# Kernel optimization log

Hardware: AMD Instinct MI355X
Metric: run time of the kernel (lower is better)

The kernel has to match this reference:

```python
import jax, jax.numpy as jnp
import numpy as np

N_NODES = 100000
NEG_SLOPE = 0.2  # PyG GATConv default leaky_relu slope


def gat_conv(x, src, dst, W, a_src, a_dst, b, concat):
    # x: [N, F_in], W: [F_in, H*C], a_src/a_dst: [H, C], b: [H*C] or [C]
    N = x.shape[0]
    H, C = a_src.shape
    h = (x @ W).reshape(N, H, C)                       # [N, H, C]
    alpha_s = jnp.einsum('nhc,hc->nh', h, a_src)       # [N, H]
    alpha_d = jnp.einsum('nhc,hc->nh', h, a_dst)       # [N, H]
    e = jax.nn.leaky_relu(alpha_s[src] + alpha_d[dst], NEG_SLOPE)  # [E, H]
    # edge-softmax grouped by destination node (numerically stable)
    e_max = jax.ops.segment_max(e, dst, num_segments=N)            # [N, H]
    e_exp = jnp.exp(e - e_max[dst])
    denom = jax.ops.segment_sum(e_exp, dst, num_segments=N)        # [N, H]
    alpha = e_exp / (denom[dst] + 1e-16)                           # [E, H]
    msg = h[src] * alpha[:, :, None]                               # [E, H, C]
    out = jax.ops.segment_sum(msg, dst, num_segments=N)            # [N, H, C]
    out = out.reshape(N, H * C) if concat else out.mean(axis=1)
    return out + b


def setup_inputs() -> dict:
    key = jax.random.key(0)
    ks = jax.random.split(key, 12)
    in_dim, hidden, heads, out_dim = 512, 128, 4, 64
    c1 = hidden // heads   # 32 per-head channels, concat -> hidden
    c2 = hidden            # 128 per-head channels, mean over heads
    E = 600000
    x = jax.random.normal(ks[0], (N_NODES, in_dim), dtype=jnp.float32)
    edge_index = jax.random.randint(ks[1], (2, E), 0, N_NODES, dtype=jnp.int64)
    s = 0.1
    return {
        'x': x,
        'edge_index': edge_index,
        'W1': jax.random.normal(ks[2], (in_dim, heads * c1), dtype=jnp.float32) * s,
        'a_src1': jax.random.normal(ks[3], (heads, c1), dtype=jnp.float32) * s,
        'a_dst1': jax.random.normal(ks[4], (heads, c1), dtype=jnp.float32) * s,
        'b1': jnp.zeros((heads * c1,), dtype=jnp.float32),
        'W2': jax.random.normal(ks[5], (hidden, heads * c2), dtype=jnp.float32) * s,
        'a_src2': jax.random.normal(ks[6], (heads, c2), dtype=jnp.float32) * s,
        'a_dst2': jax.random.normal(ks[7], (heads, c2), dtype=jnp.float32) * s,
        'b2': jnp.zeros((c2,), dtype=jnp.float32),
        'W_lin': jax.random.normal(ks[8], (hidden, out_dim), dtype=jnp.float32) * s,
        'b_lin': jnp.zeros((out_dim,), dtype=jnp.float32),
    }


def reference(x, edge_index, W1, a_src1, a_dst1, b1, W2, a_src2, a_dst2, b2, W_lin, b_lin):
    N = x.shape[0]
    # add self-loops (PyG GATConv default add_self_loops=True)
    loops = jnp.arange(N, dtype=edge_index.dtype)
    src = jnp.concatenate([edge_index[0], loops])
    dst = jnp.concatenate([edge_index[1], loops])
    # dropout layers are identity at inference (training=False)
    h = gat_conv(x, src, dst, W1, a_src1, a_dst1, b1, concat=True)
    h = jax.nn.elu(h)
    embeddings = gat_conv(h, src, dst, W2, a_src2, a_dst2, b2, concat=False)
    out = embeddings @ W_lin + b_lin
    return out, embeddings
```

## Files before the change

kernel.cpp:

```cpp
#include <hip/hip_runtime.h>
#include <hip/hip_bf16.h>

typedef __hip_bfloat16 bf16;
typedef unsigned short u16;
typedef unsigned int u32;
typedef u16 u16x8 __attribute__((ext_vector_type(8)));
typedef __bf16 bf16x8 __attribute__((ext_vector_type(8)));
typedef float f32x4 __attribute__((ext_vector_type(4)));

__device__ __forceinline__ float tof(float x) { return x; }
__device__ __forceinline__ float tof(bf16 x) { return __bfloat162float(x); }
__device__ __forceinline__ bf16 tobf(float x) { return __float2bfloat16(x); }

__device__ __forceinline__ u16 f2bf(float x) {
    unsigned u = __builtin_bit_cast(unsigned, x);
    u += 0x7fffu + ((u >> 16) & 1u);
    return (u16)(u >> 16);
}
__device__ __forceinline__ float bf2f(u16 h) {
    return __builtin_bit_cast(float, (unsigned)h << 16);
}
__device__ __forceinline__ float bflo(u32 u) {
    return __builtin_bit_cast(float, u << 16);
}
__device__ __forceinline__ float bfhi(u32 u) {
    return __builtin_bit_cast(float, u & 0xffff0000u);
}
__device__ __forceinline__ void cstore(u16* p, float v) { *p = f2bf(v); }
__device__ __forceinline__ void cstore(float* p, float v) { *p = v; }

__global__ void tsplit_k(const float* __restrict__ W, int K, int N,
                         u16* __restrict__ hi, u16* __restrict__ lo)
{
    int i = blockIdx.x * blockDim.x + threadIdx.x;
    if (i >= K * N) return;
    int k = i / N, n = i - k * N;
    float v = W[i];
    u16 h = f2bf(v);
    hi[(long)n * K + k] = h;
    lo[(long)n * K + k] = f2bf(v - bf2f(h));
}

__global__ void tsplit2_k(const float* __restrict__ W2,
                          u16* __restrict__ hi, u16* __restrict__ lo)
{
    int i = blockIdx.x * blockDim.x + threadIdx.x;
    if (i >= 128 * 512) return;
    int c = i >> 9, o2 = i & 511;
    int hh = o2 >> 7, o = o2 & 127;
    float v = W2[i];
    u16 h = f2bf(v);
    long dsti = (long)o * 512 + hh * 128 + c;
    hi[dsti] = h;
    lo[dsti] = f2bf(v - bf2f(h));
}

__global__ void vmat_k(const float* __restrict__ W2, const float* __restrict__ as2,
                       const float* __restrict__ ad2,
                       float* __restrict__ Vs, float* __restrict__ Vd)
{
    int i = blockIdx.x * blockDim.x + threadIdx.x;
    if (i >= 512) return;
    int hh = i >> 7, c = i & 127;
    float s = 0.f, d = 0.f;
    const float* wrow = W2 + (long)c * 512 + hh * 128;
    const float* ar = as2 + hh * 128;
    const float* br = ad2 + hh * 128;
    for (int o = 0; o < 128; ++o) {
        float w = wrow[o];
        s += w * ar[o];
        d += w * br[o];
    }
    Vs[i] = s;
    Vd[i] = d;
}

template <bool SPLIT_A, typename TC>
__global__ __launch_bounds__(256) void gemm_mfma(
    const void* __restrict__ Avoid, const u16* __restrict__ Bhi,
    const u16* __restrict__ Blo, TC* __restrict__ C,
    int M, int Ntot, int K, const float* __restrict__ bias)
{
    __shared__ u16 AsHi[128 * 64];
    __shared__ u16 AsLo[SPLIT_A ? 128 * 64 : 8];
    __shared__ u16 BsHi[128 * 64];
    __shared__ u16 BsLo[128 * 64];
    const int t = threadIdx.x;
    const long bm = (long)blockIdx.y * 128;
    const int bn = blockIdx.x * 128;
    const int srow = t >> 1;
    const int skh  = t & 1;
    const int w  = t >> 6;
    const int wm = (w >> 1) * 64;
    const int wn = (w & 1) * 64;
    const int l  = t & 63;
    const int lr = l & 15;
    const int lg = l >> 4;

    f32x4 acc[4][4];
#pragma unroll
    for (int i = 0; i < 4; ++i)
#pragma unroll
        for (int j = 0; j < 4; ++j) acc[i][j] = {0.f, 0.f, 0.f, 0.f};

    for (int k0 = 0; k0 < K; k0 += 64) {
        {
            long r = bm + srow;
            bool ok = r < M;
            if (SPLIT_A) {
                const float* A = (const float*)Avoid;
                const float4* ap = (const float4*)(A + r * K + k0 + skh * 32);
#pragma unroll
                for (int c = 0; c < 4; ++c) {
                    float va[8];
                    if (ok) {
                        float4 v0 = ap[c * 2], v1 = ap[c * 2 + 1];
                        va[0] = v0.x; va[1] = v0.y; va[2] = v0.z; va[3] = v0.w;
                        va[4] = v1.x; va[5] = v1.y; va[6] = v1.z; va[7] = v1.w;
                    } else {
#pragma unroll
                        for (int j = 0; j < 8; ++j) va[j] = 0.f;
                    }
                    u16x8 hi, lo;
#pragma unroll
                    for (int j = 0; j < 8; ++j) {
                        u16 h = f2bf(va[j]);
                        hi[j] = h;
                        lo[j] = f2bf(va[j] - bf2f(h));
                    }
                    int off = srow * 128 + ((((skh * 4 + c) ^ (srow & 7))) << 4);
                    *(u16x8*)((char*)AsHi + off) = hi;
                    *(u16x8*)((char*)AsLo + off) = lo;
                }
            } else {
                const u16* A = (const u16*)Avoid;
                const u16x8* ap = (const u16x8*)(A + r * K + k0 + skh * 32);
#pragma unroll
                for (int c = 0; c < 4; ++c) {
                    u16x8 hv = {0, 0, 0, 0, 0, 0, 0, 0};
                    if (ok) hv = ap[c];
                    int off = srow * 128 + ((((skh * 4 + c) ^ (srow & 7))) << 4);
                    *(u16x8*)((char*)AsHi + off) = hv;
                }
            }
        }
        {
            const u16x8* bph = (const u16x8*)(Bhi + (long)(bn + srow) * K + k0 + skh * 32);
            const u16x8* bpl = (const u16x8*)(Blo + (long)(bn + srow) * K + k0 + skh * 32);
#pragma unroll
            for (int c = 0; c < 4; ++c) {
                int off = srow * 128 + ((((skh * 4 + c) ^ (srow & 7))) << 4);
                *(u16x8*)((char*)BsHi + off) = bph[c];
                *(u16x8*)((char*)BsLo + off) = bpl[c];
            }
        }
        __syncthreads();
#pragma unroll
        for (int ks = 0; ks < 2; ++ks) {
            bf16x8 bh[4], bl[4];
            const int chl = ks * 4 + lg;
#pragma unroll
            for (int n = 0; n < 4; ++n) {
                int col = wn + n * 16 + lr;
                int off = col * 128 + (((chl ^ (col & 7))) << 4);
                bh[n] = *(const bf16x8*)((const char*)BsHi + off);
                bl[n] = *(const bf16x8*)((const char*)BsLo + off);
            }
#pragma unroll
            for (int m = 0; m < 4; ++m) {
                int row = wm + m * 16 + lr;
                int off = row * 128 + (((chl ^ (row & 7))) << 4);
                bf16x8 ah = *(const bf16x8*)((const char*)AsHi + off);
#pragma unroll
                for (int n = 0; n < 4; ++n)
                    acc[m][n] = __builtin_amdgcn_mfma_f32_16x16x32_bf16(
                        ah, bh[n], acc[m][n], 0, 0, 0);
#pragma unroll
                for (int n = 0; n < 4; ++n)
                    acc[m][n] = __builtin_amdgcn_mfma_f32_16x16x32_bf16(
                        ah, bl[n], acc[m][n], 0, 0, 0);
                if (SPLIT_A) {
                    bf16x8 al = *(const bf16x8*)((const char*)AsLo + off);
#pragma unroll
                    for (int n = 0; n < 4; ++n)
                        acc[m][n] = __builtin_amdgcn_mfma_f32_16x16x32_bf16(
                            al, bh[n], acc[m][n], 0, 0, 0);
                }
            }
        }
        __syncthreads();
    }
#pragma unroll
    for (int m = 0; m < 4; ++m) {
        long r0 = bm + wm + m * 16 + lg * 4;
#pragma unroll
        for (int i = 0; i < 4; ++i) {
            long r = r0 + i;
            if (r < M) {
#pragma unroll
                for (int n = 0; n < 4; ++n) {
                    int col = bn + wn + n * 16 + lr;
                    float v = acc[m][n][i];
                    if (bias) v += bias[col];
                    cstore(&C[r * Ntot + col], v);
                }
            }
        }
    }
}

__global__ void alpha4_k(const bf16* __restrict__ h, const float* __restrict__ asrc,
                         const float* __restrict__ adst, float* __restrict__ out_s,
                         float* __restrict__ out_d, int N)
{
    int i = blockIdx.x * blockDim.x + threadIdx.x;
    if (i >= N * 4) return;
    int n = i >> 2, hh = i & 3;
    const bf16* row = h + (long)n * 128 + hh * 32;
    const float* av = asrc + hh * 32;
    const float* bv = adst + hh * 32;
    float s1 = 0.f, s2 = 0.f;
    for (int c = 0; c < 32; ++c) {
        float v = tof(row[c]);
        s1 += v * av[c];
        s2 += v * bv[c];
    }
    out_s[i] = s1;
    out_d[i] = s2;
}

__global__ void alpha2v_k(const bf16* __restrict__ out1b, const float* __restrict__ Vs,
                          const float* __restrict__ Vd, float* __restrict__ out_s,
                          float* __restrict__ out_d, int N)
{
    int i = blockIdx.x * blockDim.x + threadIdx.x;
    if (i >= N * 4) return;
    int n = i >> 2, hh = i & 3;
    const u32* rp = (const u32*)((const u16*)out1b + (long)n * 128);
    const float* vs = Vs + hh * 128;
    const float* vd = Vd + hh * 128;
    float s1 = 0.f, s2 = 0.f;
#pragma unroll 8
    for (int c2 = 0; c2 < 64; ++c2) {
        u32 u = rp[c2];
        float lo = bflo(u), hi = bfhi(u);
        s1 += lo * vs[c2 * 2] + hi * vs[c2 * 2 + 1];
        s2 += lo * vd[c2 * 2] + hi * vd[c2 * 2 + 1];
    }
    out_s[i] = s1;
    out_d[i] = s2;
}

__global__ void init_cnt_k(int* __restrict__ cnt, int N)
{
    int i = blockIdx.x * blockDim.x + threadIdx.x;
    if (i < N) cnt[i] = 1;
}

__global__ void hist_k(const int* __restrict__ dst, int E, int* __restrict__ cnt)
{
    int e = blockIdx.x * blockDim.x + threadIdx.x;
    if (e < E) atomicAdd(&cnt[dst[e]], 1);
}

__global__ __launch_bounds__(256) void scan_blk_k(const int* __restrict__ cnt,
                                                  int* __restrict__ row_ptr,
                                                  int* __restrict__ bsum, int N)
{
    __shared__ int s[256];
    int t = threadIdx.x;
    int i = blockIdx.x * 256 + t;
    int v = (i < N) ? cnt[i] : 0;
    s[t] = v;
    __syncthreads();
    for (int off = 1; off < 256; off <<= 1) {
        int x = (t >= off) ? s[t - off] : 0;
        __syncthreads();
        s[t] += x;
        __syncthreads();
    }
    if (i < N) row_ptr[i] = s[t] - v;
    if (t == 255) bsum[blockIdx.x] = s[255];
}

__global__ __launch_bounds__(512) void scan_top_k(const int* __restrict__ bsum,
                                                  int* __restrict__ bofs, int B)
{
    __shared__ int s[512];
    int t = threadIdx.x;
    int v = (t < B) ? bsum[t] : 0;
    s[t] = v;
    __syncthreads();
    for (int off = 1; off < 512; off <<= 1) {
        int x = (t >= off) ? s[t - off] : 0;
        __syncthreads();
        s[t] += x;
        __syncthreads();
    }
    bofs[t] = s[t] - v;
}

__global__ void add_off_k(int* __restrict__ row_ptr, const int* __restrict__ bofs,
                          int* __restrict__ wofs, int N, int Etot)
{
    int i = blockIdx.x * blockDim.x + threadIdx.x;
    if (i == 0) row_ptr[N] = Etot;
    if (i >= N) return;
    int r = row_ptr[i] + bofs[i >> 8];
    row_ptr[i] = r;
    wofs[i] = r;
}

__global__ void scatter_k(const int* __restrict__ dst, const int* __restrict__ src,
                          int E, int Etot,
                          int* __restrict__ wofs, int* __restrict__ sidx)
{
    int e = blockIdx.x * blockDim.x + threadIdx.x;
    if (e >= Etot) return;
    int d, s;
    if (e < E) { d = dst[e]; s = src[e]; }
    else       { d = e - E;  s = d; }
    int pos = atomicAdd(&wofs[d], 1);
    sidx[pos] = s;
}

__global__ void edgew_k(const int* __restrict__ row_ptr, const int* __restrict__ sidx,
                        const float* __restrict__ asv, const float* __restrict__ adv,
                        float* __restrict__ aw, float* __restrict__ invden, int N)
{
    int i = blockIdx.x * blockDim.x + threadIdx.x;
    if (i >= N * 4) return;
    int d = i >> 2, hh = i & 3;
    int beg = row_ptr[d], end = row_ptr[d + 1];
    float ad_d = adv[i];
    float m = -1e30f;
    for (int j = beg; j < end; ++j) {
        float l = asv[sidx[j] * 4 + hh] + ad_d;
        l = l > 0.f ? l : 0.2f * l;
        m = fmaxf(m, l);
    }
    float den = 0.f;
    for (int j = beg; j < end; ++j) {
        float l = asv[sidx[j] * 4 + hh] + ad_d;
        l = l > 0.f ? l : 0.2f * l;
        float w = __expf(l - m);
        den += w;
        aw[(long)j * 4 + hh] = w;
    }
    invden[i] = 1.f / (den + 1e-16f);
}

__global__ __launch_bounds__(256) void agg1_gather_k(
    const int* __restrict__ row_ptr, const int* __restrict__ sidx,
    const float* __restrict__ aw, const float* __restrict__ invden,
    const bf16* __restrict__ h1, const float* __restrict__ b1,
    bf16* __restrict__ out1b, int N)
{
    int d = blockIdx.x * 4 + (threadIdx.x >> 6);
    if (d >= N) return;
    int t = threadIdx.x & 63;
    int c0 = t * 2;
    int hh = t >> 4;
    int beg = row_ptr[d], end = row_ptr[d + 1];
    float accA = 0.f, accB = 0.f;
    for (int j = beg; j < end; ++j) {
        int s = sidx[j];
        float a = aw[(long)j * 4 + hh];
        u32 u = *(const u32*)((const u16*)h1 + (long)s * 128 + c0);
        accA += a * bflo(u);
        accB += a * bfhi(u);
    }
    float inv = invden[d * 4 + hh];
    float vA = accA * inv + b1[c0];
    float vB = accB * inv + b1[c0 + 1];
    vA = vA > 0.f ? vA : (__expf(vA) - 1.f);
    vB = vB > 0.f ? vB : (__expf(vB) - 1.f);
    u32 packed = (u32)f2bf(vA) | ((u32)f2bf(vB) << 16);
    *(u32*)((u16*)out1b + (long)d * 128 + c0) = packed;
}

__global__ __launch_bounds__(256) void agg2z_gather_k(
    const int* __restrict__ row_ptr, const int* __restrict__ sidx,
    const float* __restrict__ aw, const float* __restrict__ invden,
    const bf16* __restrict__ out1b, u16* __restrict__ Z, int N)
{
    int d = blockIdx.x * 4 + (threadIdx.x >> 6);
    if (d >= N) return;
    int t = threadIdx.x & 63;
    int c0 = t * 2;
    int beg = row_ptr[d], end = row_ptr[d + 1];
    float a0A = 0.f, a0B = 0.f, a1A = 0.f, a1B = 0.f;
    float a2A = 0.f, a2B = 0.f, a3A = 0.f, a3B = 0.f;
    for (int j = beg; j < end; ++j) {
        int s = sidx[j];
        float4 w = *(const float4*)&aw[(long)j * 4];
        u32 u = *(const u32*)((const u16*)out1b + (long)s * 128 + c0);
        float lo = bflo(u), hi = bfhi(u);
        a0A += w.x * lo; a0B += w.x * hi;
        a1A += w.y * lo; a1B += w.y * hi;
        a2A += w.z * lo; a2B += w.z * hi;
        a3A += w.w * lo; a3B += w.w * hi;
    }
    float4 inv = *(const float4*)&invden[d * 4];
    u16* zrow = Z + (long)d * 512 + c0;
    float s0A = 0.25f * inv.x * a0A, s0B = 0.25f * inv.x * a0B;
    float s1A = 0.25f * inv.y * a1A, s1B = 0.25f * inv.y * a1B;
    float s2A = 0.25f * inv.z * a2A, s2B = 0.25f * inv.z * a2B;
    float s3A = 0.25f * inv.w * a3A, s3B = 0.25f * inv.w * a3B;
    *(u32*)(zrow)       = (u32)f2bf(s0A) | ((u32)f2bf(s0B) << 16);
    *(u32*)(zrow + 128) = (u32)f2bf(s1A) | ((u32)f2bf(s1B) << 16);
    *(u32*)(zrow + 256) = (u32)f2bf(s2A) | ((u32)f2bf(s2B) << 16);
    *(u32*)(zrow + 384) = (u32)f2bf(s3A) | ((u32)f2bf(s3B) << 16);
}

__global__ __launch_bounds__(256) void final_k(const float* __restrict__ emb,
                                               const float* __restrict__ W,
                                               const float* __restrict__ bias,
                                               float* __restrict__ out, int N)
{
    __shared__ float Ws[128 * 64];
    __shared__ float Es[4][132];
    const int tid = threadIdx.x;
    for (int i = tid; i < 128 * 64; i += 256) Ws[i] = W[i];
    int node0 = blockIdx.x * 4;
    for (int i = tid; i < 512; i += 256) {
        int nn = i >> 7, c = i & 127;
        int n = node0 + nn;
        Es[nn][c] = (n < N) ? emb[(long)n * 128 + c] : 0.f;
    }
    __syncthreads();
    int nn = tid >> 6, j = tid & 63;
    int n = node0 + nn;
    if (n >= N) return;
    float acc = bias[j];
#pragma unroll 8
    for (int k = 0; k < 128; ++k) acc += Es[nn][k] * Ws[k * 64 + j];
    out[(long)n * 64 + j] = acc;
}

__global__ void diag_k(float* __restrict__ out, long n, float val)
{
    long i = (long)blockIdx.x * blockDim.x + threadIdx.x;
    if (i >= n) return;
    out[i] = val;
}

extern "C" void kernel_launch(void* const* d_in, const int* in_sizes, int n_in,
                              void* d_out, int out_size, void* d_ws, size_t ws_size,
                              hipStream_t stream)
{
    const float* x   = (const float*)d_in[0];
    const int* ei    = (const int*)d_in[1];
    const float* W1  = (const float*)d_in[2];
    const float* as1 = (const float*)d_in[3];
    const float* ad1 = (const float*)d_in[4];
    const float* b1  = (const float*)d_in[5];
    const float* W2  = (const float*)d_in[6];
    const float* as2 = (const float*)d_in[7];
    const float* ad2 = (const float*)d_in[8];
    const float* b2  = (const float*)d_in[9];
    const float* Wl  = (const float*)d_in[10];
    const float* bl  = (const float*)d_in[11];

    const int N = in_sizes[0] / 512;
    const int E = in_sizes[1] / 2;
    const int Etot = E + N;
    const int* src = ei;
    const int* dst = ei + E;

    float* outp = (float*)d_out;
    float* embp = outp + (size_t)N * 64;
    bf16* out1b = (bf16*)embp;
    float* aw = outp;

    char* wsb = (char*)d_ws;
    u16*   Z     = (u16*)wsb;
    bf16*  h1    = (bf16*)wsb;
    float* asv   = (float*)(wsb + (size_t)N * 512 * sizeof(u16));
    float* adv   = asv + (size_t)N * 4;
    float* invden = adv + (size_t)N * 4;
    int*   cnt   = (int*)(invden + (size_t)N * 4);
    int*   row_ptr = cnt + N;
    int*   wofs  = row_ptr + (N + 1);
    int*   bsum  = wofs + N;
    int*   bofs  = bsum + 512;
    int*   sidx  = bofs + 512;
    char*  pw    = (char*)(sidx + Etot);
    pw = (char*)(((uintptr_t)pw + 255) & ~(uintptr_t)255);
    u16*   w1t_hi = (u16*)pw;
    u16*   w1t_lo = w1t_hi + 128 * 512;
    u16*   w2t_hi = w1t_lo + 128 * 512;
    u16*   w2t_lo = w2t_hi + 512 * 128;
    float* Vs    = (float*)(w2t_lo + 512 * 128);
    float* Vd    = Vs + 512;
    size_t need  = (size_t)((char*)(Vd + 512) - wsb);

    dim3 blk(256);
    long n_out_total = (long)N * 192;

    if (ws_size < need) {
        float val = 100.0f + (float)(ws_size >> 20);
        diag_k<<<(int)((n_out_total + 255) / 256), blk, 0, stream>>>(outp, n_out_total, val);
        return;
    }

    const int B = (N + 255) / 256;
    const int gM = (N + 127) / 128;
    const int gAgg = (N + 3) / 4;

    tsplit_k<<<(512 * 128 + 255) / 256, blk, 0, stream>>>(W1, 512, 128, w1t_hi, w1t_lo);
    tsplit2_k<<<(128 * 512 + 255) / 256, blk, 0, stream>>>(W2, w2t_hi, w2t_lo);
    vmat_k<<<2, blk, 0, stream>>>(W2, as2, ad2, Vs, Vd);

    init_cnt_k<<<B, blk, 0, stream>>>(cnt, N);
    hist_k<<<(E + 255) / 256, blk, 0, stream>>>(dst, E, cnt);
    scan_blk_k<<<B, blk, 0, stream>>>(cnt, row_ptr, bsum, N);
    scan_top_k<<<1, 512, 0, stream>>>(bsum, bofs, B);
    add_off_k<<<B, blk, 0, stream>>>(row_ptr, bofs, wofs, N, Etot);
    scatter_k<<<(Etot + 255) / 256, blk, 0, stream>>>(dst, src, E, Etot, wofs, sidx);

    gemm_mfma<true, u16><<<dim3(1, gM), blk, 0, stream>>>(
        (const void*)x, w1t_hi, w1t_lo, (u16*)h1, N, 128, 512, nullptr);
    alpha4_k<<<(N * 4 + 255) / 256, blk, 0, stream>>>(h1, as1, ad1, asv, adv, N);
    edgew_k<<<(N * 4 + 255) / 256, blk, 0, stream>>>(row_ptr, sidx, asv, adv, aw, invden, N);
    agg1_gather_k<<<gAgg, blk, 0, stream>>>(row_ptr, sidx, aw, invden, h1, b1, out1b, N);

    alpha2v_k<<<(N * 4 + 255) / 256, blk, 0, stream>>>(out1b, Vs, Vd, asv, adv, N);
    edgew_k<<<(N * 4 + 255) / 256, blk, 0, stream>>>(row_ptr, sidx, asv, adv, aw, invden, N);
    agg2z_gather_k<<<gAgg, blk, 0, stream>>>(row_ptr, sidx, aw, invden, out1b, Z, N);
    gemm_mfma<false, float><<<dim3(1, gM), blk, 0, stream>>>(
        (const void*)Z, w2t_hi, w2t_lo, embp, N, 128, 512, b2);

    final_k<<<(N + 3) / 4, blk, 0, stream>>>(embp, Wl, bl, outp, N);
}
```

Baseline: 844.7 us.

## Fuse edge softmax into gather aggregation with online softmax per destination

Replaces the separate edge-weight kernels and gather kernels with fused per-destination kernels. Each 32-lane group computes a chunked online softmax (running max and rescaled denominator) and accumulates messages in the same pass. The layer-2 attention logits are now computed in the layer-1 epilogue, which removes alpha2v_k. This cuts the aw and invden round-trips to memory and several launches. In exchange it adds shuffle-based reductions, exp rescaling per 32-edge chunk, and uses half-wave groups with 4 channels per lane. Nontemporal stores are also added for Z and the final output.

```diff
diff --git a/kernel.cpp b/kernel.cpp
--- a/kernel.cpp
+++ b/kernel.cpp
@@ -5,12 +5,11 @@
 typedef unsigned short u16;
 typedef unsigned int u32;
 typedef u16 u16x8 __attribute__((ext_vector_type(8)));
+typedef u32 u32x2 __attribute__((ext_vector_type(2)));
 typedef __bf16 bf16x8 __attribute__((ext_vector_type(8)));
 typedef float f32x4 __attribute__((ext_vector_type(4)));
 
-__device__ __forceinline__ float tof(float x) { return x; }
 __device__ __forceinline__ float tof(bf16 x) { return __bfloat162float(x); }
-__device__ __forceinline__ bf16 tobf(float x) { return __float2bfloat16(x); }
 
 __device__ __forceinline__ u16 f2bf(float x) {
     unsigned u = __builtin_bit_cast(unsigned, x);
@@ -229,28 +228,6 @@
     out_d[i] = s2;
 }
 
-__global__ void alpha2v_k(const bf16* __restrict__ out1b, const float* __restrict__ Vs,
-                          const float* __restrict__ Vd, float* __restrict__ out_s,
-                          float* __restrict__ out_d, int N)
-{
-    int i = blockIdx.x * blockDim.x + threadIdx.x;
-    if (i >= N * 4) return;
-    int n = i >> 2, hh = i & 3;
-    const u32* rp = (const u32*)((const u16*)out1b + (long)n * 128);
-    const float* vs = Vs + hh * 128;
-    const float* vd = Vd + hh * 128;
-    float s1 = 0.f, s2 = 0.f;
-#pragma unroll 8
-    for (int c2 = 0; c2 < 64; ++c2) {
-        u32 u = rp[c2];
-        float lo = bflo(u), hi = bfhi(u);
-        s1 += lo * vs[c2 * 2] + hi * vs[c2 * 2 + 1];
-        s2 += lo * vd[c2 * 2] + hi * vd[c2 * 2 + 1];
-    }
-    out_s[i] = s1;
-    out_d[i] = s2;
-}
-
 __global__ void init_cnt_k(int* __restrict__ cnt, int N)
 {
     int i = blockIdx.x * blockDim.x + threadIdx.x;
@@ -324,93 +301,203 @@
     sidx[pos] = s;
 }
 
-__global__ void edgew_k(const int* __restrict__ row_ptr, const int* __restrict__ sidx,
-                        const float* __restrict__ asv, const float* __restrict__ adv,
-                        float* __restrict__ aw, float* __restrict__ invden, int N)
-{
-    int i = blockIdx.x * blockDim.x + threadIdx.x;
-    if (i >= N * 4) return;
-    int d = i >> 2, hh = i & 3;
+__global__ __launch_bounds__(256) void agg1f_k(
+    const int* __restrict__ row_ptr, const int* __restrict__ sidx,
+    const float* __restrict__ asv, const float* __restrict__ adv,
+    const bf16* __restrict__ h1, const float* __restrict__ b1,
+    bf16* __restrict__ out1b,
+    const float* __restrict__ Vs, const float* __restrict__ Vd,
+    float* __restrict__ asv2, float* __restrict__ adv2, int N)
+{
+    int d = blockIdx.x * 8 + (threadIdx.x >> 5);
+    if (d >= N) return;
+    int ln = threadIdx.x & 31;
     int beg = row_ptr[d], end = row_ptr[d + 1];
-    float ad_d = adv[i];
-    float m = -1e30f;
-    for (int j = beg; j < end; ++j) {
-        float l = asv[sidx[j] * 4 + hh] + ad_d;
-        l = l > 0.f ? l : 0.2f * l;
-        m = fmaxf(m, l);
-    }
-    float den = 0.f;
-    for (int j = beg; j < end; ++j) {
-        float l = asv[sidx[j] * 4 + hh] + ad_d;
-        l = l > 0.f ? l : 0.2f * l;
-        float w = __expf(l - m);
-        den += w;
-        aw[(long)j * 4 + hh] = w;
-    }
-    invden[i] = 1.f / (den + 1e-16f);
-}
-
-__global__ __launch_bounds__(256) void agg1_gather_k(
+    float4 advd = *(const float4*)&adv[d * 4];
+    float mx = -1e30f, my = -1e30f, mz = -1e30f, mw = -1e30f;
+    float dnx = 0.f, dny = 0.f, dnz = 0.f, dnw = 0.f;
+    int hh = ln >> 3;
+    int c0 = ln * 4;
+    float a0 = 0.f, a1 = 0.f, a2 = 0.f, a3 = 0.f;
+    for (int j0 = beg; j0 < end; j0 += 32) {
+        int jj = j0 + ln;
+        bool valid = jj < end;
+        int s_e = valid ? sidx[jj] : 0;
+        float lx = -1e30f, ly = -1e30f, lz = -1e30f, lw = -1e30f;
+        if (valid) {
+            float4 av = *(const float4*)&asv[s_e * 4];
+            lx = av.x + advd.x; lx = lx > 0.f ? lx : 0.2f * lx;
+            ly = av.y + advd.y; ly = ly > 0.f ? ly : 0.2f * ly;
+            lz = av.z + advd.z; lz = lz > 0.f ? lz : 0.2f * lz;
+            lw = av.w + advd.w; lw = lw > 0.f ? lw : 0.2f * lw;
+        }
+        float cx = lx, cy = ly, cz = lz, cw = lw;
+#pragma unroll
+        for (int off = 16; off; off >>= 1) {
+            cx = fmaxf(cx, __shfl_xor(cx, off, 32));
+            cy = fmaxf(cy, __shfl_xor(cy, off, 32));
+            cz = fmaxf(cz, __shfl_xor(cz, off, 32));
+            cw = fmaxf(cw, __shfl_xor(cw, off, 32));
+        }
+        float nx = fmaxf(mx, cx), ny = fmaxf(my, cy);
+        float nz = fmaxf(mz, cz), nw = fmaxf(mw, cw);
+        float rx = __expf(mx - nx), ry = __expf(my - ny);
+        float rz = __expf(mz - nz), rw = __expf(mw - nw);
+        mx = nx; my = ny; mz = nz; mw = nw;
+        float wx = valid ? __expf(lx - nx) : 0.f;
+        float wy = valid ? __expf(ly - ny) : 0.f;
+        float wz = valid ? __expf(lz - nz) : 0.f;
+        float ww = valid ? __expf(lw - nw) : 0.f;
+        float sx = wx, sy = wy, sz = wz, sw = ww;
+#pragma unroll
+        for (int off = 16; off; off >>= 1) {
+            sx += __shfl_xor(sx, off, 32);
+            sy += __shfl_xor(sy, off, 32);
+            sz += __shfl_xor(sz, off, 32);
+            sw += __shfl_xor(sw, off, 32);
+        }
+        dnx = dnx * rx + sx; dny = dny * ry + sy;
+        dnz = dnz * rz + sz; dnw = dnw * rw + sw;
+        float rh = hh == 0 ? rx : hh == 1 ? ry : hh == 2 ? rz : rw;
+        a0 *= rh; a1 *= rh; a2 *= rh; a3 *= rh;
+        int cnt = min(32, end - j0);
+        for (int k = 0; k < cnt; ++k) {
+            int sk = __shfl(s_e, k, 32);
+            float bx = __shfl(wx, k, 32);
+            float by = __shfl(wy, k, 32);
+            float bz = __shfl(wz, k, 32);
+            float bw = __shfl(ww, k, 32);
+            float wk = hh == 0 ? bx : hh == 1 ? by : hh == 2 ? bz : bw;
+            u32x2 u = *(const u32x2*)((const u16*)h1 + (long)sk * 128 + c0);
+            a0 += wk * bflo(u.x); a1 += wk * bfhi(u.x);
+            a2 += wk * bflo(u.y); a3 += wk * bfhi(u.y);
+        }
+    }
+    float dh = hh == 0 ? dnx : hh == 1 ? dny : hh == 2 ? dnz : dnw;
+    float inv = 1.f / (dh + 1e-16f);
+    float4 bv = *(const float4*)&b1[c0];
+    float v0 = a0 * inv + bv.x;
+    float v1 = a1 * inv + bv.y;
+    float v2 = a2 * inv + bv.z;
+    float v3 = a3 * inv + bv.w;
+    v0 = v0 > 0.f ? v0 : (__expf(v0) - 1.f);
+    v1 = v1 > 0.f ? v1 : (__expf(v1) - 1.f);
+    v2 = v2 > 0.f ? v2 : (__expf(v2) - 1.f);
+    v3 = v3 > 0.f ? v3 : (__expf(v3) - 1.f);
+    u16 q0 = f2bf(v0), q1 = f2bf(v1), q2 = f2bf(v2), q3 = f2bf(v3);
+    u32x2 pv;
+    pv.x = (u32)q0 | ((u32)q1 << 16);
+    pv.y = (u32)q2 | ((u32)q3 << 16);
+    *(u32x2*)((u16*)out1b + (long)d * 128 + c0) = pv;
+    float f0 = bf2f(q0), f1 = bf2f(q1), f2 = bf2f(q2), f3 = bf2f(q3);
+#pragma unroll
+    for (int h = 0; h < 4; ++h) {
+        float4 vs = *(const float4*)&Vs[h * 128 + c0];
+        float4 vd = *(const float4*)&Vd[h * 128 + c0];
+        float s = f0 * vs.x + f1 * vs.y + f2 * vs.z + f3 * vs.w;
+        float t2 = f0 * vd.x + f1 * vd.y + f2 * vd.z + f3 * vd.w;
+#pragma unroll
+        for (int off = 16; off; off >>= 1) {
+            s += __shfl_xor(s, off, 32);
+            t2 += __shfl_xor(t2, off, 32);
+        }
+        if (ln == 0) { asv2[d * 4 + h] = s; adv2[d * 4 + h] = t2; }
+    }
+}
+
+__global__ __launch_bounds__(256) void agg2f_k(
     const int* __restrict__ row_ptr, const int* __restrict__ sidx,
-    const float* __restrict__ aw, const float* __restrict__ invden,
-    const bf16* __restrict__ h1, const float* __restrict__ b1,
-    bf16* __restrict__ out1b, int N)
-{
-    int d = blockIdx.x * 4 + (threadIdx.x >> 6);
+    const float* __restrict__ asv, const float* __restrict__ adv,
+    const bf16* __restrict__ out1b, u16* __restrict__ Z, int N)
+{
+    int d = blockIdx.x * 8 + (threadIdx.x >> 5);
     if (d >= N) return;
-    int t = threadIdx.x & 63;
-    int c0 = t * 2;
-    int hh = t >> 4;
+    int ln = threadIdx.x & 31;
+    int c0 = ln * 4;
     int beg = row_ptr[d], end = row_ptr[d + 1];
-    float accA = 0.f, accB = 0.f;
-    for (int j = beg; j < end; ++j) {
-        int s = sidx[j];
-        float a = aw[(long)j * 4 + hh];
-        u32 u = *(const u32*)((const u16*)h1 + (long)s * 128 + c0);
-        accA += a * bflo(u);
-        accB += a * bfhi(u);
-    }
-    float inv = invden[d * 4 + hh];
-    float vA = accA * inv + b1[c0];
-    float vB = accB * inv + b1[c0 + 1];
-    vA = vA > 0.f ? vA : (__expf(vA) - 1.f);
-    vB = vB > 0.f ? vB : (__expf(vB) - 1.f);
-    u32 packed = (u32)f2bf(vA) | ((u32)f2bf(vB) << 16);
-    *(u32*)((u16*)out1b + (long)d * 128 + c0) = packed;
-}
-
-__global__ __launch_bounds__(256) void agg2z_gather_k(
-    const int* __restrict__ row_ptr, const int* __restrict__ sidx,
-    const float* __restrict__ aw, const float* __restrict__ invden,
-    const bf16* __restrict__ out1b, u16* __restrict__ Z, int N)
-{
-    int d = blockIdx.x * 4 + (threadIdx.x >> 6);
-    if (d >= N) return;
-    int t = threadIdx.x & 63;
-    int c0 = t * 2;
-    int beg = row_ptr[d], end = row_ptr[d + 1];
-    float a0A = 0.f, a0B = 0.f, a1A = 0.f, a1B = 0.f;
-    float a2A = 0.f, a2B = 0.f, a3A = 0.f, a3B = 0.f;
-    for (int j = beg; j < end; ++j) {
-        int s = sidx[j];
-        float4 w = *(const float4*)&aw[(long)j * 4];
-        u32 u = *(const u32*)((const u16*)out1b + (long)s * 128 + c0);
-        float lo = bflo(u), hi = bfhi(u);
-        a0A += w.x * lo; a0B += w.x * hi;
-        a1A += w.y * lo; a1B += w.y * hi;
-        a2A += w.z * lo; a2B += w.z * hi;
-        a3A += w.w * lo; a3B += w.w * hi;
-    }
-    float4 inv = *(const float4*)&invden[d * 4];
+    float4 advd = *(const float4*)&adv[d * 4];
+    float mx = -1e30f, my = -1e30f, mz = -1e30f, mw = -1e30f;
+    float dnx = 0.f, dny = 0.f, dnz = 0.f, dnw = 0.f;
+    float h0c0 = 0.f, h0c1 = 0.f, h0c2 = 0.f, h0c3 = 0.f;
+    float h1c0 = 0.f, h1c1 = 0.f, h1c2 = 0.f, h1c3 = 0.f;
+    float h2c0 = 0.f, h2c1 = 0.f, h2c2 = 0.f, h2c3 = 0.f;
+    float h3c0 = 0.f, h3c1 = 0.f, h3c2 = 0.f, h3c3 = 0.f;
+    for (int j0 = beg; j0 < end; j0 += 32) {
+        int jj = j0 + ln;
+        bool valid = jj < end;
+        int s_e = valid ? sidx[jj] : 0;
+        float lx = -1e30f, ly = -1e30f, lz = -1e30f, lw = -1e30f;
+        if (valid) {
+            float4 av = *(const float4*)&asv[s_e * 4];
+            lx = av.x + advd.x; lx = lx > 0.f ? lx : 0.2f * lx;
+            ly = av.y + advd.y; ly = ly > 0.f ? ly : 0.2f * ly;
+            lz = av.z + advd.z; lz = lz > 0.f ? lz : 0.2f * lz;
+            lw = av.w + advd.w; lw = lw > 0.f ? lw : 0.2f * lw;
+        }
+        float cx = lx, cy = ly, cz = lz, cw = lw;
+#pragma unroll
+        for (int off = 16; off; off >>= 1) {
+            cx = fmaxf(cx, __shfl_xor(cx, off, 32));
+            cy = fmaxf(cy, __shfl_xor(cy, off, 32));
+            cz = fmaxf(cz, __shfl_xor(cz, off, 32));
+            cw = fmaxf(cw, __shfl_xor(cw, off, 32));
+        }
+        float nx = fmaxf(mx, cx), ny = fmaxf(my, cy);
+        float nz = fmaxf(mz, cz), nw = fmaxf(mw, cw);
+        float rx = __expf(mx - nx), ry = __expf(my - ny);
+        float rz = __expf(mz - nz), rw = __expf(mw - nw);
+        mx = nx; my = ny; mz = nz; mw = nw;
+        float wx = valid ? __expf(lx - nx) : 0.f;
+        float wy = valid ? __expf(ly - ny) : 0.f;
+        float wz = valid ? __expf(lz - nz) : 0.f;
+        float ww = valid ? __expf(lw - nw) : 0.f;
+        float sx = wx, sy = wy, sz = wz, sw = ww;
+#pragma unroll
+        for (int off = 16; off; off >>= 1) {
+            sx += __shfl_xor(sx, off, 32);
+            sy += __shfl_xor(sy, off, 32);
+            sz += __shfl_xor(sz, off, 32);
+            sw += __shfl_xor(sw, off, 32);
+        }
+        dnx = dnx * rx + sx; dny = dny * ry + sy;
+        dnz = dnz * rz + sz; dnw = dnw * rw + sw;
+        h0c0 *= rx; h0c1 *= rx; h0c2 *= rx; h0c3 *= rx;
+        h1c0 *= ry; h1c1 *= ry; h1c2 *= ry; h1c3 *= ry;
+        h2c0 *= rz; h2c1 *= rz; h2c2 *= rz; h2c3 *= rz;
+        h3c0 *= rw; h3c1 *= rw; h3c2 *= rw; h3c3 *= rw;
+        int cnt = min(32, end - j0);
+        for (int k = 0; k < cnt; ++k) {
+            int sk = __shfl(s_e, k, 32);
+            float bx = __shfl(wx, k, 32);
+            float by = __shfl(wy, k, 32);
+            float bz = __shfl(wz, k, 32);
+            float bw = __shfl(ww, k, 32);
+            u32x2 u = *(const u32x2*)((const u16*)out1b + (long)sk * 128 + c0);
+            float e0 = bflo(u.x), e1 = bfhi(u.x), e2 = bflo(u.y), e3 = bfhi(u.y);
+            h0c0 += bx * e0; h0c1 += bx * e1; h0c2 += bx * e2; h0c3 += bx * e3;
+            h1c0 += by * e0; h1c1 += by * e1; h1c2 += by * e2; h1c3 += by * e3;
+            h2c0 += bz * e0; h2c1 += bz * e1; h2c2 += bz * e2; h2c3 += bz * e3;
+            h3c0 += bw * e0; h3c1 += bw * e1; h3c2 += bw * e2; h3c3 += bw * e3;
+        }
+    }
+    float ix = 0.25f / (dnx + 1e-16f);
+    float iy = 0.25f / (dny + 1e-16f);
+    float iz = 0.25f / (dnz + 1e-16f);
+    float iw = 0.25f / (dnw + 1e-16f);
     u16* zrow = Z + (long)d * 512 + c0;
-    float s0A = 0.25f * inv.x * a0A, s0B = 0.25f * inv.x * a0B;
-    float s1A = 0.25f * inv.y * a1A, s1B = 0.25f * inv.y * a1B;
-    float s2A = 0.25f * inv.z * a2A, s2B = 0.25f * inv.z * a2B;
-    float s3A = 0.25f * inv.w * a3A, s3B = 0.25f * inv.w * a3B;
-    *(u32*)(zrow)       = (u32)f2bf(s0A) | ((u32)f2bf(s0B) << 16);
-    *(u32*)(zrow + 128) = (u32)f2bf(s1A) | ((u32)f2bf(s1B) << 16);
-    *(u32*)(zrow + 256) = (u32)f2bf(s2A) | ((u32)f2bf(s2B) << 16);
-    *(u32*)(zrow + 384) = (u32)f2bf(s3A) | ((u32)f2bf(s3B) << 16);
+    u32x2 p0, p1, p2, p3;
+    p0.x = (u32)f2bf(h0c0 * ix) | ((u32)f2bf(h0c1 * ix) << 16);
+    p0.y = (u32)f2bf(h0c2 * ix) | ((u32)f2bf(h0c3 * ix) << 16);
+    p1.x = (u32)f2bf(h1c0 * iy) | ((u32)f2bf(h1c1 * iy) << 16);
+    p1.y = (u32)f2bf(h1c2 * iy) | ((u32)f2bf(h1c3 * iy) << 16);
+    p2.x = (u32)f2bf(h2c0 * iz) | ((u32)f2bf(h2c1 * iz) << 16);
+    p2.y = (u32)f2bf(h2c2 * iz) | ((u32)f2bf(h2c3 * iz) << 16);
+    p3.x = (u32)f2bf(h3c0 * iw) | ((u32)f2bf(h3c1 * iw) << 16);
+    p3.y = (u32)f2bf(h3c2 * iw) | ((u32)f2bf(h3c3 * iw) << 16);
+    __builtin_nontemporal_store(p0, (u32x2*)(zrow));
+    __builtin_nontemporal_store(p1, (u32x2*)(zrow + 128));
+    __builtin_nontemporal_store(p2, (u32x2*)(zrow + 256));
+    __builtin_nontemporal_store(p3, (u32x2*)(zrow + 384));
 }
 
 __global__ __launch_bounds__(256) void final_k(const float* __restrict__ emb,
@@ -435,7 +522,7 @@
     float acc = bias[j];
 #pragma unroll 8
     for (int k = 0; k < 128; ++k) acc += Es[nn][k] * Ws[k * 64 + j];
-    out[(long)n * 64 + j] = acc;
+    __builtin_nontemporal_store(acc, &out[(long)n * 64 + j]);
 }
 
 __global__ void diag_k(float* __restrict__ out, long n, float val)
@@ -471,15 +558,15 @@
     float* outp = (float*)d_out;
     float* embp = outp + (size_t)N * 64;
     bf16* out1b = (bf16*)embp;
-    float* aw = outp;
 
     char* wsb = (char*)d_ws;
     u16*   Z     = (u16*)wsb;
     bf16*  h1    = (bf16*)wsb;
     float* asv   = (float*)(wsb + (size_t)N * 512 * sizeof(u16));
     float* adv   = asv + (size_t)N * 4;
-    float* invden = adv + (size_t)N * 4;
-    int*   cnt   = (int*)(invden + (size_t)N * 4);
+    float* asv2  = adv + (size_t)N * 4;
+    float* adv2  = asv2 + (size_t)N * 4;
+    int*   cnt   = (int*)(adv2 + (size_t)N * 4);
     int*   row_ptr = cnt + N;
     int*   wofs  = row_ptr + (N + 1);
     int*   bsum  = wofs + N;
@@ -506,7 +593,7 @@
 
     const int B = (N + 255) / 256;
     const int gM = (N + 127) / 128;
-    const int gAgg = (N + 3) / 4;
+    const int gAgg = (N + 7) / 8;
 
     tsplit_k<<<(512 * 128 + 255) / 256, blk, 0, stream>>>(W1, 512, 128, w1t_hi, w1t_lo);
     tsplit2_k<<<(128 * 512 + 255) / 256, blk, 0, stream>>>(W2, w2t_hi, w2t_lo);
@@ -522,12 +609,10 @@
     gemm_mfma<true, u16><<<dim3(1, gM), blk, 0, stream>>>(
         (const void*)x, w1t_hi, w1t_lo, (u16*)h1, N, 128, 512, nullptr);
     alpha4_k<<<(N * 4 + 255) / 256, blk, 0, stream>>>(h1, as1, ad1, asv, adv, N);
-    edgew_k<<<(N * 4 + 255) / 256, blk, 0, stream>>>(row_ptr, sidx, asv, adv, aw, invden, N);
-    agg1_gather_k<<<gAgg, blk, 0, stream>>>(row_ptr, sidx, aw, invden, h1, b1, out1b, N);
-
-    alpha2v_k<<<(N * 4 + 255) / 256, blk, 0, stream>>>(out1b, Vs, Vd, asv, adv, N);
-    edgew_k<<<(N * 4 + 255) / 256, blk, 0, stream>>>(row_ptr, sidx, asv, adv, aw, invden, N);
-    agg2z_gather_k<<<gAgg, blk, 0, stream>>>(row_ptr, sidx, aw, invden, out1b, Z, N);
+    agg1f_k<<<gAgg, blk, 0, stream>>>(row_ptr, sidx, asv, adv, h1, b1, out1b,
+                                      Vs, Vd, asv2, adv2, N);
+
+    agg2f_k<<<gAgg, blk, 0, stream>>>(row_ptr, sidx, asv2, adv2, out1b, Z, N);
     gemm_mfma<false, float><<<dim3(1, gM), blk, 0, stream>>>(
         (const void*)Z, w2t_hi, w2t_lo, embp, N, 128, 512, b2);
 
```

New measurement: 745.9 us. 1.13x faster.
